# Performance work log

Measured on AMD Instinct MI355X. Metric: run time of the kernel, lower is better.

## Reference

```python
import jax, jax.numpy as jnp
import numpy as np

N_GRAPHS = 10000
NODES_PER_GRAPH = 200
N_NODES = N_GRAPHS * NODES_PER_GRAPH
D = 128

def setup_inputs() -> dict:
    key = jax.random.key(0)
    ks = jax.random.split(key, 4)
    self_feats = jax.random.normal(ks[0], (N_NODES, D), dtype=jnp.float32)
    graph_size = jnp.full((N_GRAPHS,), NODES_PER_GRAPH, dtype=jnp.int64)
    # MLP params: Dense(256) on 2*D=256 input, Dense(128), Dense(1)
    def glorot(k, shape):
        fan_in, fan_out = shape
        lim = np.sqrt(6.0 / (fan_in + fan_out)).astype(np.float32)
        return jax.random.uniform(k, shape, jnp.float32, -lim, lim)
    W0 = glorot(ks[1], (2 * D, 256))
    W1 = glorot(ks[2], (256, 128))
    W2 = glorot(ks[3], (128, 1))
    return {
        "self_feats": self_feats, "graph_size": graph_size,
        "W0": W0, "b0": jnp.zeros((256,), jnp.float32),
        "W1": W1, "b1": jnp.zeros((128,), jnp.float32),
        "W2": W2, "b2": jnp.zeros((1,), jnp.float32),
    }

def reference(self_feats, graph_size, W0, b0, W1, b1, W2, b2):
    G = graph_size.shape[0]
    N = self_feats.shape[0]
    # segment ids from per-graph sizes (equivalent to the cumsum slicing loop)
    seg = jnp.repeat(jnp.arange(G), graph_size, total_repeat_length=N)
    counts = graph_size.astype(self_feats.dtype)[:, None]
    mean_feats = jax.ops.segment_sum(self_feats, seg, num_segments=G) / counts  # [G, D]
    max_feats = jax.ops.segment_max(self_feats, seg, num_segments=G)           # [G, D]
    pooled = jnp.concatenate([mean_feats, max_feats], axis=1)                   # [G, 2D]
    h = jax.nn.relu(pooled @ W0 + b0)
    h = jax.nn.relu(h @ W1 + b1)
    return jax.nn.sigmoid(h @ W2 + b2)  # [G, 1]
```

## Files before the change

kernel.cpp:

```cpp
#include <hip/hip_runtime.h>
#include <hip/hip_bf16.h>
#include <math.h>

#define GPB 8

typedef float fx4 __attribute__((ext_vector_type(4)));

__global__ __launch_bounds__(256) void fused_pool_mlp_kernel(
    const float* __restrict__ feats, const int* __restrict__ gsize,
    const float* __restrict__ W0, const float* __restrict__ b0,
    const float* __restrict__ W1, const float* __restrict__ b1,
    const float* __restrict__ W2, const float* __restrict__ b2,
    float* __restrict__ out, int G)
{
    __shared__ __align__(16) float4 X4[GPB * 64];
    __shared__ __align__(16) float  H0[GPB * 256];
    __shared__ __align__(16) float  H1[GPB * 128];
    __shared__ int soff[GPB], ssize[GPB];
    __shared__ int red[4];

    int t    = threadIdx.x;
    int lane = t & 63;
    int wave = t >> 6;
    int g0   = blockIdx.x * GPB;

    int partial = 0;
    {
        const int4* gs4 = (const int4*)gsize;
        int n4 = g0 >> 2;
        for (int i = t; i < n4; i += 256) {
            int4 v = gs4[i];
            partial += v.x + v.y + v.z + v.w;
        }
    }
    #pragma unroll
    for (int d = 32; d > 0; d >>= 1) partial += __shfl_xor(partial, d);
    if (lane == 0) red[wave] = partial;
    __syncthreads();
    if (t == 0) {
        int base = red[0] + red[1] + red[2] + red[3];
        #pragma unroll
        for (int q = 0; q < GPB; ++q) {
            int g = g0 + q;
            int n = (g < G) ? gsize[g] : 0;
            soff[q] = base; ssize[q] = n; base += n;
        }
    }
    __syncthreads();

    const float NEG = -3.402823466e38f;
    #pragma unroll
    for (int qq = 0; qq < GPB / 4; ++qq) {
        int gi = wave * (GPB / 4) + qq;
        int n  = ssize[gi];
        float4 outv = make_float4(0.f, 0.f, 0.f, 0.f);
        if (n > 0) {
            const fx4* p = (const fx4*)feats + (size_t)soff[gi] * 32;
            float sx = 0.f, sy = 0.f, sz = 0.f, sw = 0.f;
            float mx = NEG, my = NEG, mz = NEG, mw = NEG;
            int npairs = n >> 1;
            int i = 0;
            for (; i + 8 <= npairs; i += 8) {
                fx4 v[8];
                #pragma unroll
                for (int u = 0; u < 8; ++u)
                    v[u] = p[(size_t)(i + u) * 64 + lane];
                #pragma unroll
                for (int u = 0; u < 8; ++u) {
                    sx += v[u].x; sy += v[u].y; sz += v[u].z; sw += v[u].w;
                    mx = fmaxf(mx, v[u].x); my = fmaxf(my, v[u].y);
                    mz = fmaxf(mz, v[u].z); mw = fmaxf(mw, v[u].w);
                }
            }
            for (; i < npairs; ++i) {
                fx4 v = p[(size_t)i * 64 + lane];
                sx += v.x; sy += v.y; sz += v.z; sw += v.w;
                mx = fmaxf(mx, v.x); my = fmaxf(my, v.y);
                mz = fmaxf(mz, v.z); mw = fmaxf(mw, v.w);
            }
            if ((n & 1) && lane < 32) {
                fx4 v = p[(size_t)(n - 1) * 32 + lane];
                sx += v.x; sy += v.y; sz += v.z; sw += v.w;
                mx = fmaxf(mx, v.x); my = fmaxf(my, v.y);
                mz = fmaxf(mz, v.z); mw = fmaxf(mw, v.w);
            }
            sx += __shfl_xor(sx, 32); sy += __shfl_xor(sy, 32);
            sz += __shfl_xor(sz, 32); sw += __shfl_xor(sw, 32);
            mx = fmaxf(mx, __shfl_xor(mx, 32)); my = fmaxf(my, __shfl_xor(my, 32));
            mz = fmaxf(mz, __shfl_xor(mz, 32)); mw = fmaxf(mw, __shfl_xor(mw, 32));
            if (lane < 32) {
                float invn = 1.0f / (float)n;
                outv = make_float4(sx * invn, sy * invn, sz * invn, sw * invn);
            } else {
                outv = make_float4(mx, my, mz, mw);
            }
        }
        X4[gi * 64 + lane] = outv;
    }
    __syncthreads();

    {
        float acc[GPB];
        float bb = b0[t];
        #pragma unroll
        for (int q = 0; q < GPB; ++q) acc[q] = bb;
        for (int k4 = 0; k4 < 64; ++k4) {
            const float* Wk = W0 + (size_t)k4 * 1024;
            float w0v = Wk[t], w1v = Wk[256 + t], w2v = Wk[512 + t], w3v = Wk[768 + t];
            #pragma unroll
            for (int q = 0; q < GPB; ++q) {
                float4 x = X4[q * 64 + k4];
                acc[q] = fmaf(x.x, w0v, acc[q]);
                acc[q] = fmaf(x.y, w1v, acc[q]);
                acc[q] = fmaf(x.z, w2v, acc[q]);
                acc[q] = fmaf(x.w, w3v, acc[q]);
            }
        }
        #pragma unroll
        for (int q = 0; q < GPB; ++q)
            H0[q * 256 + t] = fmaxf(acc[q], 0.f);
    }
    __syncthreads();

    {
        int jl = t & 127;
        int gh = t >> 7;
        float acc[4];
        float bb = b1[jl];
        #pragma unroll
        for (int q = 0; q < 4; ++q) acc[q] = bb;
        const float4* H04 = (const float4*)H0;
        for (int k4 = 0; k4 < 64; ++k4) {
            const float* Wk = W1 + (size_t)k4 * 512;
            float w0v = Wk[jl],       w1v = Wk[128 + jl];
            float w2v = Wk[256 + jl], w3v = Wk[384 + jl];
            #pragma unroll
            for (int q = 0; q < 4; ++q) {
                float4 x = H04[(gh * 4 + q) * 64 + k4];
                acc[q] = fmaf(x.x, w0v, acc[q]);
                acc[q] = fmaf(x.y, w1v, acc[q]);
                acc[q] = fmaf(x.z, w2v, acc[q]);
                acc[q] = fmaf(x.w, w3v, acc[q]);
            }
        }
        #pragma unroll
        for (int q = 0; q < 4; ++q)
            H1[(gh * 4 + q) * 128 + jl] = fmaxf(acc[q], 0.f);
    }
    __syncthreads();

    {
        int gi  = t >> 5;
        int sub = t & 31;
        float acc = 0.f;
        #pragma unroll
        for (int kk = 0; kk < 4; ++kk) {
            int k = sub + kk * 32;
            acc = fmaf(H1[gi * 128 + k], W2[k], acc);
        }
        acc += __shfl_xor(acc, 16);
        acc += __shfl_xor(acc, 8);
        acc += __shfl_xor(acc, 4);
        acc += __shfl_xor(acc, 2);
        acc += __shfl_xor(acc, 1);
        int g = g0 + gi;
        if (sub == 0 && g < G)
            out[g] = 1.0f / (1.0f + expf(-(acc + b2[0])));
    }
}

extern "C" void kernel_launch(void* const* d_in, const int* in_sizes, int n_in,
                              void* d_out, int out_size, void* d_ws, size_t ws_size,
                              hipStream_t stream) {
    const float* feats = (const float*)d_in[0];
    const int*   gsize = (const int*)d_in[1];
    const float* W0 = (const float*)d_in[2];
    const float* b0 = (const float*)d_in[3];
    const float* W1 = (const float*)d_in[4];
    const float* b1 = (const float*)d_in[5];
    const float* W2 = (const float*)d_in[6];
    const float* b2 = (const float*)d_in[7];
    float* out = (float*)d_out;

    int G = in_sizes[1];
    int blocks = (G + GPB - 1) / GPB;
    fused_pool_mlp_kernel<<<blocks, 256, 0, stream>>>(
        feats, gsize, W0, b0, W1, b1, W2, b2, out, G);
}
```

Before: 226.8 us.

## Overlap second-half pooling loads with first-half MLP layers inside each block

Each block's eight graphs are split into two halves of four. After the first half is pooled, the streaming loads for the second half are interleaved with the first half's Dense(256) and Dense(128) compute, so memory latency is hidden behind FMA work. The second half's MLP then runs afterward. All feature loads also switch to nontemporal hints to avoid polluting cache. This adds code complexity, register pressure and an extra barrier.

Result: slower. 242.0 us (+6.7%).

```diff
diff --git a/kernel.cpp b/kernel.cpp
--- a/kernel.cpp
+++ b/kernel.cpp
@@ -5,6 +5,13 @@
 #define GPB 8
 
 typedef float fx4 __attribute__((ext_vector_type(4)));
+
+#define POOL_CONSUME(vv)                                        \
+    do {                                                        \
+        sx += (vv).x; sy += (vv).y; sz += (vv).z; sw += (vv).w; \
+        mx = fmaxf(mx, (vv).x); my = fmaxf(my, (vv).y);         \
+        mz = fmaxf(mz, (vv).z); mw = fmaxf(mw, (vv).w);         \
+    } while (0)
 
 __global__ __launch_bounds__(256) void fused_pool_mlp_kernel(
     const float* __restrict__ feats, const int* __restrict__ gsize,
@@ -49,9 +56,9 @@
     __syncthreads();
 
     const float NEG = -3.402823466e38f;
-    #pragma unroll
-    for (int qq = 0; qq < GPB / 4; ++qq) {
-        int gi = wave * (GPB / 4) + qq;
+
+    {
+        int gi = wave;
         int n  = ssize[gi];
         float4 outv = make_float4(0.f, 0.f, 0.f, 0.f);
         if (n > 0) {
@@ -64,25 +71,17 @@
                 fx4 v[8];
                 #pragma unroll
                 for (int u = 0; u < 8; ++u)
-                    v[u] = p[(size_t)(i + u) * 64 + lane];
-                #pragma unroll
-                for (int u = 0; u < 8; ++u) {
-                    sx += v[u].x; sy += v[u].y; sz += v[u].z; sw += v[u].w;
-                    mx = fmaxf(mx, v[u].x); my = fmaxf(my, v[u].y);
-                    mz = fmaxf(mz, v[u].z); mw = fmaxf(mw, v[u].w);
-                }
+                    v[u] = __builtin_nontemporal_load(p + (size_t)(i + u) * 64 + lane);
+                #pragma unroll
+                for (int u = 0; u < 8; ++u) POOL_CONSUME(v[u]);
             }
             for (; i < npairs; ++i) {
-                fx4 v = p[(size_t)i * 64 + lane];
-                sx += v.x; sy += v.y; sz += v.z; sw += v.w;
-                mx = fmaxf(mx, v.x); my = fmaxf(my, v.y);
-                mz = fmaxf(mz, v.z); mw = fmaxf(mw, v.w);
+                fx4 v = __builtin_nontemporal_load(p + (size_t)i * 64 + lane);
+                POOL_CONSUME(v);
             }
             if ((n & 1) && lane < 32) {
-                fx4 v = p[(size_t)(n - 1) * 32 + lane];
-                sx += v.x; sy += v.y; sz += v.z; sw += v.w;
-                mx = fmaxf(mx, v.x); my = fmaxf(my, v.y);
-                mz = fmaxf(mz, v.z); mw = fmaxf(mw, v.w);
+                fx4 v = __builtin_nontemporal_load(p + (size_t)(n - 1) * 32 + lane);
+                POOL_CONSUME(v);
             }
             sx += __shfl_xor(sx, 32); sy += __shfl_xor(sy, 32);
             sz += __shfl_xor(sz, 32); sw += __shfl_xor(sw, 32);
@@ -100,52 +99,176 @@
     __syncthreads();
 
     {
-        float acc[GPB];
+        int gi = 4 + wave;
+        int n  = ssize[gi];
+        const fx4* p = (const fx4*)feats + (size_t)soff[gi] * 32;
+        float sx = 0.f, sy = 0.f, sz = 0.f, sw = 0.f;
+        float mx = NEG, my = NEG, mz = NEG, mw = NEG;
+        int npairs = (n > 0) ? (n >> 1) : 0;
+        int nb     = npairs >> 3;
+        int nbw    = (nb < 12) ? nb : 12;
+        int nbpre  = nb - nbw;
+
+        for (int b = 0; b < nbpre; ++b) {
+            fx4 v[8];
+            #pragma unroll
+            for (int u = 0; u < 8; ++u)
+                v[u] = __builtin_nontemporal_load(p + (size_t)(b * 8 + u) * 64 + lane);
+            #pragma unroll
+            for (int u = 0; u < 8; ++u) POOL_CONSUME(v[u]);
+        }
+
+        float accA[4];
+        {
+            float bb = b0[t];
+            #pragma unroll
+            for (int g = 0; g < 4; ++g) accA[g] = bb;
+        }
+        #pragma unroll 1
+        for (int s = 0; s < 8; ++s) {
+            bool act = (s < nbw);
+            fx4 v[8];
+            const fx4* pb = p + (size_t)(nbpre + s) * 512 + lane;
+            if (act) {
+                #pragma unroll
+                for (int u = 0; u < 8; ++u)
+                    v[u] = __builtin_nontemporal_load(pb + (size_t)u * 64);
+            }
+            #pragma unroll
+            for (int kk = 0; kk < 8; ++kk) {
+                int k4 = s * 8 + kk;
+                const float* Wk = W0 + (size_t)k4 * 1024;
+                float w0v = Wk[t], w1v = Wk[256 + t], w2v = Wk[512 + t], w3v = Wk[768 + t];
+                #pragma unroll
+                for (int g = 0; g < 4; ++g) {
+                    float4 x = X4[g * 64 + k4];
+                    accA[g] = fmaf(x.x, w0v, accA[g]);
+                    accA[g] = fmaf(x.y, w1v, accA[g]);
+                    accA[g] = fmaf(x.z, w2v, accA[g]);
+                    accA[g] = fmaf(x.w, w3v, accA[g]);
+                }
+            }
+            if (act) {
+                #pragma unroll
+                for (int u = 0; u < 8; ++u) POOL_CONSUME(v[u]);
+            }
+        }
+        #pragma unroll
+        for (int g = 0; g < 4; ++g) H0[g * 256 + t] = fmaxf(accA[g], 0.f);
+        __syncthreads();
+
+        int jl = t & 127;
+        int gh = t >> 7;
+        float accB[2];
+        {
+            float bb = b1[jl];
+            accB[0] = bb; accB[1] = bb;
+        }
+        const float4* H04 = (const float4*)H0;
+        #pragma unroll 1
+        for (int s = 8; s < 12; ++s) {
+            bool act = (s < nbw);
+            fx4 v[8];
+            const fx4* pb = p + (size_t)(nbpre + s) * 512 + lane;
+            if (act) {
+                #pragma unroll
+                for (int u = 0; u < 8; ++u)
+                    v[u] = __builtin_nontemporal_load(pb + (size_t)u * 64);
+            }
+            #pragma unroll
+            for (int kk = 0; kk < 16; ++kk) {
+                int k4 = (s - 8) * 16 + kk;
+                const float* Wk = W1 + (size_t)k4 * 512;
+                float w0v = Wk[jl],       w1v = Wk[128 + jl];
+                float w2v = Wk[256 + jl], w3v = Wk[384 + jl];
+                #pragma unroll
+                for (int g = 0; g < 2; ++g) {
+                    float4 x = H04[(gh * 2 + g) * 64 + k4];
+                    accB[g] = fmaf(x.x, w0v, accB[g]);
+                    accB[g] = fmaf(x.y, w1v, accB[g]);
+                    accB[g] = fmaf(x.z, w2v, accB[g]);
+                    accB[g] = fmaf(x.w, w3v, accB[g]);
+                }
+            }
+            if (act) {
+                #pragma unroll
+                for (int u = 0; u < 8; ++u) POOL_CONSUME(v[u]);
+            }
+        }
+        #pragma unroll
+        for (int g = 0; g < 2; ++g)
+            H1[(gh * 2 + g) * 128 + jl] = fmaxf(accB[g], 0.f);
+
+        for (int i = nb * 8; i < npairs; ++i) {
+            fx4 v = __builtin_nontemporal_load(p + (size_t)i * 64 + lane);
+            POOL_CONSUME(v);
+        }
+        if (n > 0 && (n & 1) && lane < 32) {
+            fx4 v = __builtin_nontemporal_load(p + (size_t)(n - 1) * 32 + lane);
+            POOL_CONSUME(v);
+        }
+        float4 outv = make_float4(0.f, 0.f, 0.f, 0.f);
+        if (n > 0) {
+            sx += __shfl_xor(sx, 32); sy += __shfl_xor(sy, 32);
+            sz += __shfl_xor(sz, 32); sw += __shfl_xor(sw, 32);
+            mx = fmaxf(mx, __shfl_xor(mx, 32)); my = fmaxf(my, __shfl_xor(my, 32));
+            mz = fmaxf(mz, __shfl_xor(mz, 32)); mw = fmaxf(mw, __shfl_xor(mw, 32));
+            if (lane < 32) {
+                float invn = 1.0f / (float)n;
+                outv = make_float4(sx * invn, sy * invn, sz * invn, sw * invn);
+            } else {
+                outv = make_float4(mx, my, mz, mw);
+            }
+        }
+        X4[gi * 64 + lane] = outv;
+    }
+    __syncthreads();
+
+    {
+        float acc[4];
         float bb = b0[t];
         #pragma unroll
-        for (int q = 0; q < GPB; ++q) acc[q] = bb;
+        for (int g = 0; g < 4; ++g) acc[g] = bb;
         for (int k4 = 0; k4 < 64; ++k4) {
             const float* Wk = W0 + (size_t)k4 * 1024;
             float w0v = Wk[t], w1v = Wk[256 + t], w2v = Wk[512 + t], w3v = Wk[768 + t];
             #pragma unroll
-            for (int q = 0; q < GPB; ++q) {
-                float4 x = X4[q * 64 + k4];
-                acc[q] = fmaf(x.x, w0v, acc[q]);
-                acc[q] = fmaf(x.y, w1v, acc[q]);
-                acc[q] = fmaf(x.z, w2v, acc[q]);
-                acc[q] = fmaf(x.w, w3v, acc[q]);
-            }
-        }
-        #pragma unroll
-        for (int q = 0; q < GPB; ++q)
-            H0[q * 256 + t] = fmaxf(acc[q], 0.f);
-    }
-    __syncthreads();
-
+            for (int g = 0; g < 4; ++g) {
+                float4 x = X4[(4 + g) * 64 + k4];
+                acc[g] = fmaf(x.x, w0v, acc[g]);
+                acc[g] = fmaf(x.y, w1v, acc[g]);
+                acc[g] = fmaf(x.z, w2v, acc[g]);
+                acc[g] = fmaf(x.w, w3v, acc[g]);
+            }
+        }
+        #pragma unroll
+        for (int g = 0; g < 4; ++g)
+            H0[(4 + g) * 256 + t] = fmaxf(acc[g], 0.f);
+    }
+    __syncthreads();
     {
         int jl = t & 127;
         int gh = t >> 7;
-        float acc[4];
+        float acc[2];
         float bb = b1[jl];
-        #pragma unroll
-        for (int q = 0; q < 4; ++q) acc[q] = bb;
+        acc[0] = bb; acc[1] = bb;
         const float4* H04 = (const float4*)H0;
         for (int k4 = 0; k4 < 64; ++k4) {
             const float* Wk = W1 + (size_t)k4 * 512;
             float w0v = Wk[jl],       w1v = Wk[128 + jl];
             float w2v = Wk[256 + jl], w3v = Wk[384 + jl];
             #pragma unroll
-            for (int q = 0; q < 4; ++q) {
-                float4 x = H04[(gh * 4 + q) * 64 + k4];
-                acc[q] = fmaf(x.x, w0v, acc[q]);
-                acc[q] = fmaf(x.y, w1v, acc[q]);
-                acc[q] = fmaf(x.z, w2v, acc[q]);
-                acc[q] = fmaf(x.w, w3v, acc[q]);
-            }
-        }
-        #pragma unroll
-        for (int q = 0; q < 4; ++q)
-            H1[(gh * 4 + q) * 128 + jl] = fmaxf(acc[q], 0.f);
+            for (int g = 0; g < 2; ++g) {
+                float4 x = H04[(4 + gh * 2 + g) * 64 + k4];
+                acc[g] = fmaf(x.x, w0v, acc[g]);
+                acc[g] = fmaf(x.y, w1v, acc[g]);
+                acc[g] = fmaf(x.z, w2v, acc[g]);
+                acc[g] = fmaf(x.w, w3v, acc[g]);
+            }
+        }
+        #pragma unroll
+        for (int g = 0; g < 2; ++g)
+            H1[(4 + gh * 2 + g) * 128 + jl] = fmaxf(acc[g], 0.f);
     }
     __syncthreads();
 
```

## Process more graphs per block to amortize MLP weight reads; use nontemporal feature loads

Applied to the files above, without the earlier changes.

Each block now handles 20 graphs with 512 threads instead of 8 graphs with 256. W0 and W1 are therefore fetched from L2 far fewer times across the grid, which cuts cache traffic that competes with the feature stream. The dense layers are remapped so two or four thread groups each cover a slice of the graphs, and waves stride over graphs in the pooling phase. Feature loads become nontemporal so the one-pass stream does not pollute the cache. The trade-offs are an uneven pooling load (some waves handle 3 graphs, others 2), more LDS per block, and fewer blocks to spread across the CUs.

Result: faster. 191.4 us (-15.6%).

```diff
diff --git a/kernel.cpp b/kernel.cpp
--- a/kernel.cpp
+++ b/kernel.cpp
@@ -2,11 +2,20 @@
 #include <hip/hip_bf16.h>
 #include <math.h>
 
-#define GPB 8
+#define GPB     20
+#define THREADS 512
+#define NWAVES  8
 
 typedef float fx4 __attribute__((ext_vector_type(4)));
 
-__global__ __launch_bounds__(256) void fused_pool_mlp_kernel(
+#define POOL_CONSUME(vv)                                        \
+    do {                                                        \
+        sx += (vv).x; sy += (vv).y; sz += (vv).z; sw += (vv).w; \
+        mx = fmaxf(mx, (vv).x); my = fmaxf(my, (vv).y);         \
+        mz = fmaxf(mz, (vv).z); mw = fmaxf(mw, (vv).w);         \
+    } while (0)
+
+__global__ __launch_bounds__(THREADS, 4) void fused_pool_mlp_kernel(
     const float* __restrict__ feats, const int* __restrict__ gsize,
     const float* __restrict__ W0, const float* __restrict__ b0,
     const float* __restrict__ W1, const float* __restrict__ b1,
@@ -17,7 +26,7 @@
     __shared__ __align__(16) float  H0[GPB * 256];
     __shared__ __align__(16) float  H1[GPB * 128];
     __shared__ int soff[GPB], ssize[GPB];
-    __shared__ int red[4];
+    __shared__ int red[NWAVES];
 
     int t    = threadIdx.x;
     int lane = t & 63;
@@ -28,7 +37,7 @@
     {
         const int4* gs4 = (const int4*)gsize;
         int n4 = g0 >> 2;
-        for (int i = t; i < n4; i += 256) {
+        for (int i = t; i < n4; i += THREADS) {
             int4 v = gs4[i];
             partial += v.x + v.y + v.z + v.w;
         }
@@ -38,8 +47,9 @@
     if (lane == 0) red[wave] = partial;
     __syncthreads();
     if (t == 0) {
-        int base = red[0] + red[1] + red[2] + red[3];
+        int base = 0;
         #pragma unroll
+        for (int w = 0; w < NWAVES; ++w) base += red[w];
         for (int q = 0; q < GPB; ++q) {
             int g = g0 + q;
             int n = (g < G) ? gsize[g] : 0;
@@ -49,10 +59,9 @@
     __syncthreads();
 
     const float NEG = -3.402823466e38f;
-    #pragma unroll
-    for (int qq = 0; qq < GPB / 4; ++qq) {
-        int gi = wave * (GPB / 4) + qq;
-        int n  = ssize[gi];
+    #pragma unroll 1
+    for (int gi = wave; gi < GPB; gi += NWAVES) {
+        int n = ssize[gi];
         float4 outv = make_float4(0.f, 0.f, 0.f, 0.f);
         if (n > 0) {
             const fx4* p = (const fx4*)feats + (size_t)soff[gi] * 32;
@@ -64,25 +73,17 @@
                 fx4 v[8];
                 #pragma unroll
                 for (int u = 0; u < 8; ++u)
-                    v[u] = p[(size_t)(i + u) * 64 + lane];
+                    v[u] = __builtin_nontemporal_load(p + (size_t)(i + u) * 64 + lane);
                 #pragma unroll
-                for (int u = 0; u < 8; ++u) {
-                    sx += v[u].x; sy += v[u].y; sz += v[u].z; sw += v[u].w;
-                    mx = fmaxf(mx, v[u].x); my = fmaxf(my, v[u].y);
-                    mz = fmaxf(mz, v[u].z); mw = fmaxf(mw, v[u].w);
-                }
+                for (int u = 0; u < 8; ++u) POOL_CONSUME(v[u]);
             }
             for (; i < npairs; ++i) {
-                fx4 v = p[(size_t)i * 64 + lane];
-                sx += v.x; sy += v.y; sz += v.z; sw += v.w;
-                mx = fmaxf(mx, v.x); my = fmaxf(my, v.y);
-                mz = fmaxf(mz, v.z); mw = fmaxf(mw, v.w);
+                fx4 v = __builtin_nontemporal_load(p + (size_t)i * 64 + lane);
+                POOL_CONSUME(v);
             }
             if ((n & 1) && lane < 32) {
-                fx4 v = p[(size_t)(n - 1) * 32 + lane];
-                sx += v.x; sy += v.y; sz += v.z; sw += v.w;
-                mx = fmaxf(mx, v.x); my = fmaxf(my, v.y);
-                mz = fmaxf(mz, v.z); mw = fmaxf(mw, v.w);
+                fx4 v = __builtin_nontemporal_load(p + (size_t)(n - 1) * 32 + lane);
+                POOL_CONSUME(v);
             }
             sx += __shfl_xor(sx, 32); sy += __shfl_xor(sy, 32);
             sz += __shfl_xor(sz, 32); sw += __shfl_xor(sw, 32);
@@ -100,16 +101,18 @@
     __syncthreads();
 
     {
-        float acc[GPB];
-        float bb = b0[t];
+        int j  = t & 255;
+        int gq = t >> 8;
+        float acc[10];
+        float bb = b0[j];
         #pragma unroll
-        for (int q = 0; q < GPB; ++q) acc[q] = bb;
+        for (int q = 0; q < 10; ++q) acc[q] = bb;
         for (int k4 = 0; k4 < 64; ++k4) {
             const float* Wk = W0 + (size_t)k4 * 1024;
-            float w0v = Wk[t], w1v = Wk[256 + t], w2v = Wk[512 + t], w3v = Wk[768 + t];
+            float w0v = Wk[j], w1v = Wk[256 + j], w2v = Wk[512 + j], w3v = Wk[768 + j];
             #pragma unroll
-            for (int q = 0; q < GPB; ++q) {
-                float4 x = X4[q * 64 + k4];
+            for (int q = 0; q < 10; ++q) {
+                float4 x = X4[(gq * 10 + q) * 64 + k4];
                 acc[q] = fmaf(x.x, w0v, acc[q]);
                 acc[q] = fmaf(x.y, w1v, acc[q]);
                 acc[q] = fmaf(x.z, w2v, acc[q]);
@@ -117,26 +120,26 @@
             }
         }
         #pragma unroll
-        for (int q = 0; q < GPB; ++q)
-            H0[q * 256 + t] = fmaxf(acc[q], 0.f);
+        for (int q = 0; q < 10; ++q)
+            H0[(gq * 10 + q) * 256 + j] = fmaxf(acc[q], 0.f);
     }
     __syncthreads();
 
     {
-        int jl = t & 127;
-        int gh = t >> 7;
-        float acc[4];
-        float bb = b1[jl];
+        int j  = t & 127;
+        int gq = t >> 7;
+        float acc[5];
+        float bb = b1[j];
         #pragma unroll
-        for (int q = 0; q < 4; ++q) acc[q] = bb;
+        for (int q = 0; q < 5; ++q) acc[q] = bb;
         const float4* H04 = (const float4*)H0;
         for (int k4 = 0; k4 < 64; ++k4) {
             const float* Wk = W1 + (size_t)k4 * 512;
-            float w0v = Wk[jl],       w1v = Wk[128 + jl];
-            float w2v = Wk[256 + jl], w3v = Wk[384 + jl];
+            float w0v = Wk[j],       w1v = Wk[128 + j];
+            float w2v = Wk[256 + j], w3v = Wk[384 + j];
             #pragma unroll
-            for (int q = 0; q < 4; ++q) {
-                float4 x = H04[(gh * 4 + q) * 64 + k4];
+            for (int q = 0; q < 5; ++q) {
+                float4 x = H04[(gq * 5 + q) * 64 + k4];
                 acc[q] = fmaf(x.x, w0v, acc[q]);
                 acc[q] = fmaf(x.y, w1v, acc[q]);
                 acc[q] = fmaf(x.z, w2v, acc[q]);
@@ -144,28 +147,29 @@
             }
         }
         #pragma unroll
-        for (int q = 0; q < 4; ++q)
-            H1[(gh * 4 + q) * 128 + jl] = fmaxf(acc[q], 0.f);
+        for (int q = 0; q < 5; ++q)
+            H1[(gq * 5 + q) * 128 + j] = fmaxf(acc[q], 0.f);
     }
     __syncthreads();
 
     {
-        int gi  = t >> 5;
-        int sub = t & 31;
-        float acc = 0.f;
-        #pragma unroll
-        for (int kk = 0; kk < 4; ++kk) {
-            int k = sub + kk * 32;
-            acc = fmaf(H1[gi * 128 + k], W2[k], acc);
+        int gi  = t >> 4;
+        int sub = t & 15;
+        if (gi < GPB) {
+            float acc = 0.f;
+            #pragma unroll
+            for (int kk = 0; kk < 8; ++kk) {
+                int k = sub + kk * 16;
+                acc = fmaf(H1[gi * 128 + k], W2[k], acc);
+            }
+            acc += __shfl_xor(acc, 8);
+            acc += __shfl_xor(acc, 4);
+            acc += __shfl_xor(acc, 2);
+            acc += __shfl_xor(acc, 1);
+            int g = g0 + gi;
+            if (sub == 0 && g < G)
+                out[g] = 1.0f / (1.0f + expf(-(acc + b2[0])));
         }
-        acc += __shfl_xor(acc, 16);
-        acc += __shfl_xor(acc, 8);
-        acc += __shfl_xor(acc, 4);
-        acc += __shfl_xor(acc, 2);
-        acc += __shfl_xor(acc, 1);
-        int g = g0 + gi;
-        if (sub == 0 && g < G)
-            out[g] = 1.0f / (1.0f + expf(-(acc + b2[0])));
     }
 }
 
@@ -184,6 +188,6 @@
 
     int G = in_sizes[1];
     int blocks = (G + GPB - 1) / GPB;
-    fused_pool_mlp_kernel<<<blocks, 256, 0, stream>>>(
+    fused_pool_mlp_kernel<<<blocks, THREADS, 0, stream>>>(
         feats, gsize, W0, b0, W1, b1, W2, b2, out, G);
 }
```
